# Kernel tuning notes

Measured on AMD Instinct MI355X. Metric: run time of the kernel, lower is better.

The kernel has to match this reference:

```python
import jax, jax.numpy as jnp
import numpy as np

Q_LAYERS = 2

def _cnot(s, c, t):
    # s: [N,2,2,2,2]; wire w lives on axis w+1. Here t = c+1 always.
    s0 = jnp.take(s, 0, axis=c + 1)          # control=0 slice (axis removed)
    s1 = jnp.take(s, 1, axis=c + 1)          # control=1 slice
    t_ax = t + 1 - (1 if t > c else 0)       # target axis after removal
    s1 = jnp.flip(s1, axis=t_ax)             # X on target
    return jnp.stack([s0, s1], axis=c + 1)

def _ry(s, w, theta):
    a = w + 1
    co, si = jnp.cos(theta / 2), jnp.sin(theta / 2)
    s0 = jnp.take(s, 0, axis=a)
    s1 = jnp.take(s, 1, axis=a)
    return jnp.stack([co * s0 - si * s1, si * s0 + co * s1], axis=a)

def _quantum_features(x2d):
    # x2d: [B,28,28] -> per 2x2 patch angles [p00,p01,p10,p11]
    B = x2d.shape[0]
    p = x2d.reshape(B, 14, 2, 14, 2).transpose(0, 1, 3, 2, 4).reshape(-1, 4)  # [N,4]
    half = 0.5 * p
    c_, s_ = jnp.cos(half), jnp.sin(half)
    # RY(a_i)|0> product state, real amplitudes throughout (RY/CNOT only)
    state = (jnp.stack([c_[:, 0], s_[:, 0]], -1)[:, :, None, None, None]
             * jnp.stack([c_[:, 1], s_[:, 1]], -1)[:, None, :, None, None]
             * jnp.stack([c_[:, 2], s_[:, 2]], -1)[:, None, None, :, None]
             * jnp.stack([c_[:, 3], s_[:, 3]], -1)[:, None, None, None, :])
    qpi4 = jnp.asarray(np.pi / 4, dtype=state.dtype)
    for _ in range(Q_LAYERS):
        for w in range(3):
            state = _cnot(state, w, w + 1)
        state = _ry(state, 3, qpi4)
    probs = state * state
    z = jnp.stack([jnp.take(probs, 0, axis=w + 1).sum((1, 2, 3))
                   - jnp.take(probs, 1, axis=w + 1).sum((1, 2, 3))
                   for w in range(4)], axis=-1)      # [N,4]
    return z.reshape(B, 14 * 14 * 4)

def setup_inputs() -> dict:
    key = jax.random.key(0)
    ks = jax.random.split(key, 5)
    B = 8192
    return {
        'x': jax.random.normal(ks[0], (B, 1, 28, 28), dtype=jnp.float32),
        'conv_w': jax.random.normal(ks[1], (4, 1, 2, 2), dtype=jnp.float32) * 0.5,
        'conv_b': jax.random.normal(ks[2], (4,), dtype=jnp.float32) * 0.1,
        'fc_w': jax.random.normal(ks[3], (10, 1568), dtype=jnp.float32) * 0.02,
        'fc_b': jax.random.normal(ks[4], (10,), dtype=jnp.float32) * 0.02,
    }

def reference(x, conv_w, conv_b, fc_w, fc_b):
    B = x.shape[0]
    conv = jax.lax.conv_general_dilated(
        x, conv_w, window_strides=(2, 2), padding='VALID',
        dimension_numbers=('NCHW', 'OIHW', 'NCHW')) + conv_b[None, :, None, None]
    conv_flat = conv.reshape(B, -1)                   # [B, 4*14*14]
    q_feat = _quantum_features(x[:, 0])               # [B, 4*14*14]
    fused = jnp.concatenate([conv_flat, q_feat], axis=1)
    logits = fused @ fc_w.T + fc_b
    return jax.nn.log_softmax(logits, axis=-1)
```

## Files before the change

### kernel.cpp

```cpp
#include <hip/hip_runtime.h>


typedef _Float16 f16x8 __attribute__((ext_vector_type(8)));
typedef float    f32x4 __attribute__((ext_vector_type(4)));
typedef unsigned int u32x4 __attribute__((ext_vector_type(4)));

#define XSTRIDE 788

__global__ __launch_bounds__(512, 4) void quanv_mfma(
    const float* __restrict__ x,
    const float* __restrict__ conv_w,
    const float* __restrict__ conv_b,
    const float* __restrict__ fc_w,
    const float* __restrict__ fc_b,
    float* __restrict__ out,
    int B)
{
    __shared__ __align__(16) float xl[16 * XSTRIDE];
    __shared__ float red[8][16][16];

    const int tid  = threadIdx.x;
    const int wid  = tid >> 6;
    const int lane = tid & 63;
    const int l15  = lane & 15;
    const int slot = lane >> 4;
    const int b0   = blockIdx.x * 16;

    const int   o   = l15;
    const int   oc  = (o < 10) ? o : 9;
    const float msk = (o < 10) ? 1.f : 0.f;
    const float* wr = fc_w + oc * 1568;

    f16x8 bw[7];
#pragma unroll
    for (int j = 0; j < 7; ++j) {
        const int g = wid + (j << 3);
        if (g < 49) {
            const int p = (g << 2) + slot;
            const float w0 = wr[p]       * msk;
            const float w1 = wr[196 + p] * msk;
            const float w2 = wr[392 + p] * msk;
            const float w3 = wr[588 + p] * msk;
            const float4 wq = *reinterpret_cast<const float4*>(wr + 784 + p * 4);
            u32x4 wu;
            wu[0] = __builtin_bit_cast(unsigned int, __builtin_amdgcn_cvt_pkrtz(w0, w1));
            wu[1] = __builtin_bit_cast(unsigned int, __builtin_amdgcn_cvt_pkrtz(w2, w3));
            wu[2] = __builtin_bit_cast(unsigned int, __builtin_amdgcn_cvt_pkrtz(wq.x * msk, wq.y * msk));
            wu[3] = __builtin_bit_cast(unsigned int, __builtin_amdgcn_cvt_pkrtz(wq.z * msk, wq.w * msk));
            bw[j] = __builtin_bit_cast(f16x8, wu);
        } else {
            u32x4 z = {0u, 0u, 0u, 0u};
            bw[j] = __builtin_bit_cast(f16x8, z);
        }
    }

    float cw[16], cb[4];
#pragma unroll
    for (int i = 0; i < 16; ++i) cw[i] = conv_w[i];
#pragma unroll
    for (int i = 0; i < 4; ++i) cb[i] = conv_b[i];

    {
        const float* xg = x + (size_t)b0 * 784;
        for (int i = tid; i < 3136; i += 512) {
            const float4 v = *reinterpret_cast<const float4*>(xg + 4 * i);
            const int img = i / 196;
            const int w   = (i - img * 196) * 4;
            *reinterpret_cast<float4*>(&xl[img * XSTRIDE + w]) = v;
        }
    }
    __syncthreads();

    const float* xim = &xl[l15 * XSTRIDE];
    f32x4 acc = {0.f, 0.f, 0.f, 0.f};

#pragma unroll
    for (int j = 0; j < 7; ++j) {
        const int g = wid + (j << 3);
        if (g < 49) {
            const int p   = (g << 2) + slot;
            const int pi  = p / 14;
            const int pj  = p - pi * 14;
            const int off = pi * 56 + pj * 2;

            const float2 r0 = *reinterpret_cast<const float2*>(xim + off);
            const float2 r1 = *reinterpret_cast<const float2*>(xim + off + 28);
            const float x00 = r0.x, x01 = r0.y, x10 = r1.x, x11 = r1.y;

            const float ft0 = fmaf(x00, cw[0],  fmaf(x01, cw[1],  fmaf(x10, cw[2],  fmaf(x11, cw[3],  cb[0]))));
            const float ft1 = fmaf(x00, cw[4],  fmaf(x01, cw[5],  fmaf(x10, cw[6],  fmaf(x11, cw[7],  cb[1]))));
            const float ft2 = fmaf(x00, cw[8],  fmaf(x01, cw[9],  fmaf(x10, cw[10], fmaf(x11, cw[11], cb[2]))));
            const float ft3 = fmaf(x00, cw[12], fmaf(x01, cw[13], fmaf(x10, cw[14], fmaf(x11, cw[15], cb[3]))));

            const float c0 = __cosf(x00);
            const float c1 = __cosf(x01);
            const float c2 = __cosf(x10);
            const float s3 = __sinf(x11);
            const float c3 = __cosf(x11);
            const float t  = c0 * c2;
            const float u  = c1 * c3;
            const float z3 = 0.5f * ((u - s3) - t * (u + s3));

            u32x4 au;
            au[0] = __builtin_bit_cast(unsigned int, __builtin_amdgcn_cvt_pkrtz(ft0, ft1));
            au[1] = __builtin_bit_cast(unsigned int, __builtin_amdgcn_cvt_pkrtz(ft2, ft3));
            au[2] = __builtin_bit_cast(unsigned int, __builtin_amdgcn_cvt_pkrtz(c0, c1));
            au[3] = __builtin_bit_cast(unsigned int, __builtin_amdgcn_cvt_pkrtz(t, z3));
            const f16x8 a = __builtin_bit_cast(f16x8, au);

            acc = __builtin_amdgcn_mfma_f32_16x16x32_f16(a, bw[j], acc, 0, 0, 0);
        }
    }

#pragma unroll
    for (int r = 0; r < 4; ++r)
        red[wid][slot * 4 + r][l15] = acc[r];
    __syncthreads();

    if (tid < 256) {
        const int row = tid >> 4, col = tid & 15;
        float s = 0.f;
#pragma unroll
        for (int w = 0; w < 8; ++w) s += red[w][row][col];
        red[0][row][col] = s;
    }
    __syncthreads();

    if (tid < 16) {
        const int im = tid;
        if (b0 + im < B) {
            float lg[10];
#pragma unroll
            for (int j = 0; j < 10; ++j) lg[j] = red[0][im][j] + fc_b[j];
            float mx = lg[0];
#pragma unroll
            for (int j = 1; j < 10; ++j) mx = fmaxf(mx, lg[j]);
            float se = 0.f;
#pragma unroll
            for (int j = 0; j < 10; ++j) se += __expf(lg[j] - mx);
            const float lse = __logf(se) + mx;
            float* op = out + (size_t)(b0 + im) * 10;
#pragma unroll
            for (int j = 0; j < 10; ++j) op[j] = lg[j] - lse;
        }
    }
}

extern "C" void kernel_launch(void* const* d_in, const int* in_sizes, int n_in,
                              void* d_out, int out_size, void* d_ws, size_t ws_size,
                              hipStream_t stream) {
    const float* x      = (const float*)d_in[0];
    const float* conv_w = (const float*)d_in[1];
    const float* conv_b = (const float*)d_in[2];
    const float* fc_w   = (const float*)d_in[3];
    const float* fc_b   = (const float*)d_in[4];
    float* out = (float*)d_out;

    const int B = in_sizes[0] / 784;
    const int blocks = (B + 15) / 16;
    quanv_mfma<<<blocks, 512, 0, stream>>>(x, conv_w, conv_b, fc_w, fc_b, out, B);
}
```

Before: 21.23 us.

## Prefetch input before weight setup and use hardware sin/cos on prescaled inputs

Global loads of the 16-image tile are issued into registers before the fc weight packing, so load latency overlaps the weight conversion. Inputs are prescaled by 1/(2π) in shared memory so the native amdgcn sin/cos instructions can be called directly, with conv weights scaled by 2π to compensate. The 0.5 factor on z3 is folded into the fc weight and an fma. The patch pixels are loaded from LDS ahead of the MFMA loop, and the loop is unrolled with the tail handled only by wave 0. This raises register pressure (about 28 prefetched floats plus 14 float2 per thread) under launch_bounds(512,4), and the hardware trig path changes precision slightly.

```diff
diff --git a/kernel.cpp b/kernel.cpp
--- a/kernel.cpp
+++ b/kernel.cpp
@@ -6,6 +6,8 @@
 typedef unsigned int u32x4 __attribute__((ext_vector_type(4)));
 
 #define XSTRIDE 788
+#define INV2PI 0.15915494309189535f
+#define TWOPI  6.283185307179586f
 
 __global__ __launch_bounds__(512, 4) void quanv_mfma(
     const float* __restrict__ x,
@@ -25,6 +27,14 @@
     const int l15  = lane & 15;
     const int slot = lane >> 4;
     const int b0   = blockIdx.x * 16;
+
+    const float* xg = x + (size_t)b0 * 784;
+    float4 sv[7];
+#pragma unroll
+    for (int c = 0; c < 7; ++c) {
+        const int i = tid + (c << 9);
+        if (c < 6 || i < 3136) sv[c] = *reinterpret_cast<const float4*>(xg + 4 * i);
+    }
 
     const int   o   = l15;
     const int   oc  = (o < 10) ? o : 9;
@@ -46,7 +56,7 @@
             wu[0] = __builtin_bit_cast(unsigned int, __builtin_amdgcn_cvt_pkrtz(w0, w1));
             wu[1] = __builtin_bit_cast(unsigned int, __builtin_amdgcn_cvt_pkrtz(w2, w3));
             wu[2] = __builtin_bit_cast(unsigned int, __builtin_amdgcn_cvt_pkrtz(wq.x * msk, wq.y * msk));
-            wu[3] = __builtin_bit_cast(unsigned int, __builtin_amdgcn_cvt_pkrtz(wq.z * msk, wq.w * msk));
+            wu[3] = __builtin_bit_cast(unsigned int, __builtin_amdgcn_cvt_pkrtz(wq.z * msk, wq.w * (0.5f * msk)));
             bw[j] = __builtin_bit_cast(f16x8, wu);
         } else {
             u32x4 z = {0u, 0u, 0u, 0u};
@@ -56,61 +66,70 @@
 
     float cw[16], cb[4];
 #pragma unroll
-    for (int i = 0; i < 16; ++i) cw[i] = conv_w[i];
+    for (int i = 0; i < 16; ++i) cw[i] = conv_w[i] * TWOPI;
 #pragma unroll
     for (int i = 0; i < 4; ++i) cb[i] = conv_b[i];
 
-    {
-        const float* xg = x + (size_t)b0 * 784;
-        for (int i = tid; i < 3136; i += 512) {
-            const float4 v = *reinterpret_cast<const float4*>(xg + 4 * i);
+#pragma unroll
+    for (int c = 0; c < 7; ++c) {
+        const int i = tid + (c << 9);
+        if (c < 6 || i < 3136) {
             const int img = i / 196;
             const int w   = (i - img * 196) * 4;
+            float4 v = sv[c];
+            v.x *= INV2PI; v.y *= INV2PI; v.z *= INV2PI; v.w *= INV2PI;
             *reinterpret_cast<float4*>(&xl[img * XSTRIDE + w]) = v;
         }
     }
     __syncthreads();
 
     const float* xim = &xl[l15 * XSTRIDE];
+    float2 pxa[7], pxb[7];
+#pragma unroll
+    for (int j = 0; j < 6; ++j) {
+        const int p   = ((wid + (j << 3)) << 2) + slot;
+        const int pi  = p / 14;
+        const int pj  = p - pi * 14;
+        const int off = pi * 56 + pj * 2;
+        pxa[j] = *reinterpret_cast<const float2*>(xim + off);
+        pxb[j] = *reinterpret_cast<const float2*>(xim + off + 28);
+    }
+    if (wid == 0) {
+        const int p   = 192 + slot;
+        const int off = 13 * 56 + (p - 182) * 2;
+        pxa[6] = *reinterpret_cast<const float2*>(xim + off);
+        pxb[6] = *reinterpret_cast<const float2*>(xim + off + 28);
+    }
+
     f32x4 acc = {0.f, 0.f, 0.f, 0.f};
 
-#pragma unroll
-    for (int j = 0; j < 7; ++j) {
-        const int g = wid + (j << 3);
-        if (g < 49) {
-            const int p   = (g << 2) + slot;
-            const int pi  = p / 14;
-            const int pj  = p - pi * 14;
-            const int off = pi * 56 + pj * 2;
+#define BODY(j)                                                                 \
+    {                                                                           \
+        const float x00 = pxa[j].x, x01 = pxa[j].y;                             \
+        const float x10 = pxb[j].x, x11 = pxb[j].y;                             \
+        const float ft0 = fmaf(x00, cw[0],  fmaf(x01, cw[1],  fmaf(x10, cw[2],  fmaf(x11, cw[3],  cb[0])))); \
+        const float ft1 = fmaf(x00, cw[4],  fmaf(x01, cw[5],  fmaf(x10, cw[6],  fmaf(x11, cw[7],  cb[1])))); \
+        const float ft2 = fmaf(x00, cw[8],  fmaf(x01, cw[9],  fmaf(x10, cw[10], fmaf(x11, cw[11], cb[2])))); \
+        const float ft3 = fmaf(x00, cw[12], fmaf(x01, cw[13], fmaf(x10, cw[14], fmaf(x11, cw[15], cb[3])))); \
+        const float c0 = __builtin_amdgcn_cosf(x00);                            \
+        const float c1 = __builtin_amdgcn_cosf(x01);                            \
+        const float c2 = __builtin_amdgcn_cosf(x10);                            \
+        const float s3 = __builtin_amdgcn_sinf(x11);                            \
+        const float c3 = __builtin_amdgcn_cosf(x11);                            \
+        const float t  = c0 * c2;                                               \
+        const float u  = c1 * c3;                                               \
+        const float z3 = fmaf(-t, u + s3, u - s3);       \
+        u32x4 au;                                                               \
+        au[0] = __builtin_bit_cast(unsigned int, __builtin_amdgcn_cvt_pkrtz(ft0, ft1)); \
+        au[1] = __builtin_bit_cast(unsigned int, __builtin_amdgcn_cvt_pkrtz(ft2, ft3)); \
+        au[2] = __builtin_bit_cast(unsigned int, __builtin_amdgcn_cvt_pkrtz(c0, c1));   \
+        au[3] = __builtin_bit_cast(unsigned int, __builtin_amdgcn_cvt_pkrtz(t, z3));    \
+        acc = __builtin_amdgcn_mfma_f32_16x16x32_f16(__builtin_bit_cast(f16x8, au), bw[j], acc, 0, 0, 0); \
+    }
 
-            const float2 r0 = *reinterpret_cast<const float2*>(xim + off);
-            const float2 r1 = *reinterpret_cast<const float2*>(xim + off + 28);
-            const float x00 = r0.x, x01 = r0.y, x10 = r1.x, x11 = r1.y;
-
-            const float ft0 = fmaf(x00, cw[0],  fmaf(x01, cw[1],  fmaf(x10, cw[2],  fmaf(x11, cw[3],  cb[0]))));
-            const float ft1 = fmaf(x00, cw[4],  fmaf(x01, cw[5],  fmaf(x10, cw[6],  fmaf(x11, cw[7],  cb[1]))));
-            const float ft2 = fmaf(x00, cw[8],  fmaf(x01, cw[9],  fmaf(x10, cw[10], fmaf(x11, cw[11], cb[2]))));
-            const float ft3 = fmaf(x00, cw[12], fmaf(x01, cw[13], fmaf(x10, cw[14], fmaf(x11, cw[15], cb[3]))));
-
-            const float c0 = __cosf(x00);
-            const float c1 = __cosf(x01);
-            const float c2 = __cosf(x10);
-            const float s3 = __sinf(x11);
-            const float c3 = __cosf(x11);
-            const float t  = c0 * c2;
-            const float u  = c1 * c3;
-            const float z3 = 0.5f * ((u - s3) - t * (u + s3));
-
-            u32x4 au;
-            au[0] = __builtin_bit_cast(unsigned int, __builtin_amdgcn_cvt_pkrtz(ft0, ft1));
-            au[1] = __builtin_bit_cast(unsigned int, __builtin_amdgcn_cvt_pkrtz(ft2, ft3));
-            au[2] = __builtin_bit_cast(unsigned int, __builtin_amdgcn_cvt_pkrtz(c0, c1));
-            au[3] = __builtin_bit_cast(unsigned int, __builtin_amdgcn_cvt_pkrtz(t, z3));
-            const f16x8 a = __builtin_bit_cast(f16x8, au);
-
-            acc = __builtin_amdgcn_mfma_f32_16x16x32_f16(a, bw[j], acc, 0, 0, 0);
-        }
-    }
+    BODY(0) BODY(1) BODY(2) BODY(3) BODY(4) BODY(5)
+    if (wid == 0) BODY(6)
+#undef BODY
 
 #pragma unroll
     for (int r = 0; r < 4; ++r)
```

Result: faster. 19.59 us (-7.7%).
